# Kernel optimization log

Measured on AMD Instinct MI355X. Metric: run time of the kernel, lower is better.

Reference implementation:

```python
import jax, jax.numpy as jnp
import numpy as np

LATENT = 768
HEADS = 12
HEAD_DIM = LATENT // HEADS
FFN = 4 * LATENT


def setup_inputs() -> dict:
    key = jax.random.key(0)
    ks = jax.random.split(key, 16)
    s = 1.0 / np.sqrt(LATENT)
    inp = {
        "x": jax.random.normal(ks[0], (2, 2048, LATENT), dtype=jnp.float32),
        "Wq": jax.random.normal(ks[1], (LATENT, LATENT), dtype=jnp.float32) * s,
        "bq": jnp.zeros((LATENT,), jnp.float32),
        "Wk": jax.random.normal(ks[2], (LATENT, LATENT), dtype=jnp.float32) * s,
        "bk": jnp.zeros((LATENT,), jnp.float32),
        "Wv": jax.random.normal(ks[3], (LATENT, LATENT), dtype=jnp.float32) * s,
        "bv": jnp.zeros((LATENT,), jnp.float32),
        "Wo": jax.random.normal(ks[4], (LATENT, LATENT), dtype=jnp.float32) * s,
        "bo": jnp.zeros((LATENT,), jnp.float32),
        "ln1_g": jnp.ones((LATENT,), jnp.float32),
        "ln1_b": jnp.zeros((LATENT,), jnp.float32),
        "ln2_g": jnp.ones((LATENT,), jnp.float32),
        "ln2_b": jnp.zeros((LATENT,), jnp.float32),
        "W1": jax.random.normal(ks[5], (FFN, LATENT), dtype=jnp.float32) * s,
        "b1": jnp.zeros((FFN,), jnp.float32),
        "W2": jax.random.normal(ks[6], (LATENT, FFN), dtype=jnp.float32) * (1.0 / np.sqrt(FFN)),
        "b2": jnp.zeros((LATENT,), jnp.float32),
    }
    return inp


def _layernorm(x, g, b, eps=1e-5):
    mu = jnp.mean(x, axis=-1, keepdims=True)
    var = jnp.var(x, axis=-1, keepdims=True)
    return (x - mu) * jax.lax.rsqrt(var + eps) * g + b


def reference(x, Wq, bq, Wk, bk, Wv, bv, Wo, bo, ln1_g, ln1_b, ln2_g, ln2_b, W1, b1, W2, b2):
    b, n, d = x.shape
    # torch Linear: y = x @ W.T + bias
    Q = (x @ Wq.T + bq).reshape(b, n, HEADS, HEAD_DIM).transpose(0, 2, 1, 3)
    K = (x @ Wk.T + bk).reshape(b, n, HEADS, HEAD_DIM).transpose(0, 2, 1, 3)
    V = (x @ Wv.T + bv).reshape(b, n, HEADS, HEAD_DIM).transpose(0, 2, 1, 3)
    scores = jnp.einsum("bhqd,bhkd->bhqk", Q, K) / np.sqrt(HEAD_DIM)  # [b,h,n,n]
    weights = jax.nn.softmax(scores, axis=-1)
    attn = jnp.einsum("bhqk,bhkd->bhqd", weights, V)
    attn = attn.transpose(0, 2, 1, 3).reshape(b, n, d)
    attn = attn @ Wo.T + bo
    x = _layernorm(x + attn, ln1_g, ln1_b)
    h = jax.nn.gelu(x @ W1.T + b1, approximate=False)
    ffn = h @ W2.T + b2
    x = _layernorm(x + ffn, ln2_g, ln2_b)
    return x
```

## Files before the change

kernel.cpp:

```cpp
#include <hip/hip_runtime.h>
#include <hip/hip_bf16.h>
#include <cstddef>
#include <cstdint>

typedef __bf16 bf16_t;
typedef bf16_t bf16x8 __attribute__((ext_vector_type(8)));
typedef bf16_t bf16x4 __attribute__((ext_vector_type(4)));
typedef float f32x4 __attribute__((ext_vector_type(4)));

#define LATENT 768
#define FFN_DIM 3072
#define NTOK 4096
#define SEQ 2048
#define HEADS 12
#define HD 64

#define C2F 0.18033688011112042f

__device__ __forceinline__ void gload_lds16(const bf16_t* g, bf16_t* l) {
    __builtin_amdgcn_global_load_lds((const __attribute__((address_space(1))) void*)g,
                                     (__attribute__((address_space(3))) void*)l, 16, 0, 0);
}

struct CvtDesc {
    const float* src[7];
    bf16_t* dst[7];
    int n4[7];
    const float* bsrc[3];
    float* bdst;
};

__global__ __launch_bounds__(256) void cvt_f32_bf16(CvtDesc d) {
    int seg = blockIdx.y;
    if (seg == 7) {
        int which = blockIdx.x;
        if (which >= 3) return;
        int t = threadIdx.x;
#pragma unroll
        for (int i = 0; i < 3; ++i)
            d.bdst[which * LATENT + t + i * 256] = d.bsrc[which][t + i * 256];
        return;
    }
    int i = blockIdx.x * 256 + threadIdx.x;
    if (i >= d.n4[seg]) return;
    float4 v = ((const float4*)d.src[seg])[i];
    bf16x4 o;
    o[0] = (bf16_t)v.x; o[1] = (bf16_t)v.y; o[2] = (bf16_t)v.z; o[3] = (bf16_t)v.w;
    *(bf16x4*)&d.dst[seg][(size_t)i * 4] = o;
}

template<int EPI, int NT>
__global__ __launch_bounds__(256) void gemm128(const bf16_t* __restrict__ A,
                                               const bf16_t* __restrict__ B,
                                               const float* __restrict__ bias,
                                               void* __restrict__ Cv,
                                               int M, int N, int K) {
    __shared__ __align__(16) bf16_t As[2][128 * 32];
    __shared__ __align__(16) bf16_t Bs[2][NT * 32];
    int t = threadIdx.x;
    int w = t >> 6;
    int lane = t & 63, l16 = lane & 15, quad = lane >> 4;
    int xt = blockIdx.x + blockIdx.y;
    if (xt >= (int)gridDim.x) xt -= gridDim.x;
    int m0 = xt * 128, n0 = blockIdx.y * NT;
    int mrow0 = (w & 1) * 64, ncol0 = (w >> 1) * (NT / 2);
    const int NJ = NT / 32;

    f32x4 acc[4][NJ] = {};

    int srow = lane >> 2;
    int sseg = (lane & 3) * 8;

    auto stage = [&](int k0, int buf) {
        const bf16_t* Ag = A + (size_t)(m0 + w * 32 + srow) * K + k0 + sseg;
        gload_lds16(Ag,          &As[buf][(w * 32) * 32]);
        gload_lds16(Ag + 16 * K, &As[buf][(w * 32 + 16) * 32]);
        if (NT == 128) {
            const bf16_t* Bg = B + (size_t)(n0 + w * 32 + srow) * K + k0 + sseg;
            gload_lds16(Bg,          &Bs[buf][(w * 32) * 32]);
            gload_lds16(Bg + 16 * K, &Bs[buf][(w * 32 + 16) * 32]);
        } else {
            const bf16_t* Bg = B + (size_t)(n0 + w * 16 + srow) * K + k0 + sseg;
            gload_lds16(Bg, &Bs[buf][(w * 16) * 32]);
        }
    };

    int niter = K / 32;
    stage(0, 0);
    for (int kt = 0; kt < niter; ++kt) {
        __syncthreads();
        int cur = kt & 1;
        if (kt + 1 < niter) stage((kt + 1) * 32, cur ^ 1);

        bf16x8 a[4], b[NJ];
#pragma unroll
        for (int i = 0; i < 4; ++i)
            a[i] = *(const bf16x8*)&As[cur][(mrow0 + i * 16 + l16) * 32 + quad * 8];
#pragma unroll
        for (int j = 0; j < NJ; ++j)
            b[j] = *(const bf16x8*)&Bs[cur][(ncol0 + j * 16 + l16) * 32 + quad * 8];
#pragma unroll
        for (int i = 0; i < 4; ++i)
#pragma unroll
            for (int j = 0; j < NJ; ++j)
                acc[i][j] = __builtin_amdgcn_mfma_f32_16x16x32_bf16(a[i], b[j], acc[i][j], 0, 0, 0);
    }

    float* Cf = (float*)Cv;
    bf16_t* Cb = (bf16_t*)Cv;
#pragma unroll
    for (int j = 0; j < NJ; ++j) {
        int col = n0 + ncol0 + j * 16 + l16;
        float bvv = bias[col];
#pragma unroll
        for (int i = 0; i < 4; ++i) {
            int row0 = m0 + mrow0 + i * 16 + quad * 4;
#pragma unroll
            for (int r = 0; r < 4; ++r) {
                float v = acc[i][j][r] + bvv;
                if (EPI == 2) v = 0.5f * v * (1.0f + erff(v * 0.70710678118654752f));
                if (EPI == 3) { if (col < LATENT) v *= C2F; }
                if (EPI == 0) Cf[(size_t)(row0 + r) * N + col] = v;
                else          Cb[(size_t)(row0 + r) * N + col] = (bf16_t)v;
            }
        }
    }
}

template<int EPI>
__global__ __launch_bounds__(128) void gemm64(const bf16_t* __restrict__ A,
                                              const bf16_t* __restrict__ B,
                                              const float* __restrict__ bias,
                                              void* __restrict__ Cv,
                                              int M, int N, int K) {
    __shared__ __align__(16) bf16_t As[2][64 * 32];
    __shared__ __align__(16) bf16_t Bs[2][64 * 32];
    int t = threadIdx.x;
    int w = t >> 6;
    int lane = t & 63, l16 = lane & 15, quad = lane >> 4;
    int m0 = blockIdx.x * 64, n0 = blockIdx.y * 64;

    f32x4 acc[2][4] = {};

    int srow = lane >> 2;
    int sseg = (lane & 3) * 8;

    auto stage = [&](int k0, int buf) {
        const bf16_t* Ag = A + (size_t)(m0 + w * 32 + srow) * K + k0 + sseg;
        gload_lds16(Ag,          &As[buf][(w * 32) * 32]);
        gload_lds16(Ag + 16 * K, &As[buf][(w * 32 + 16) * 32]);
        const bf16_t* Bg = B + (size_t)(n0 + w * 32 + srow) * K + k0 + sseg;
        gload_lds16(Bg,          &Bs[buf][(w * 32) * 32]);
        gload_lds16(Bg + 16 * K, &Bs[buf][(w * 32 + 16) * 32]);
    };

    int niter = K / 32;
    stage(0, 0);
    for (int kt = 0; kt < niter; ++kt) {
        __syncthreads();
        int cur = kt & 1;
        if (kt + 1 < niter) stage((kt + 1) * 32, cur ^ 1);

        bf16x8 a[2], b[4];
#pragma unroll
        for (int i = 0; i < 2; ++i)
            a[i] = *(const bf16x8*)&As[cur][(w * 32 + i * 16 + l16) * 32 + quad * 8];
#pragma unroll
        for (int j = 0; j < 4; ++j)
            b[j] = *(const bf16x8*)&Bs[cur][(j * 16 + l16) * 32 + quad * 8];
#pragma unroll
        for (int i = 0; i < 2; ++i)
#pragma unroll
            for (int j = 0; j < 4; ++j)
                acc[i][j] = __builtin_amdgcn_mfma_f32_16x16x32_bf16(a[i], b[j], acc[i][j], 0, 0, 0);
    }

    float* Cf = (float*)Cv;
    bf16_t* Cb = (bf16_t*)Cv;
#pragma unroll
    for (int j = 0; j < 4; ++j) {
        int col = n0 + j * 16 + l16;
        float bvv = bias[col];
#pragma unroll
        for (int i = 0; i < 2; ++i) {
            int row0 = m0 + w * 32 + i * 16 + quad * 4;
#pragma unroll
            for (int r = 0; r < 4; ++r) {
                float v = acc[i][j][r] + bvv;
                if (EPI == 2) v = 0.5f * v * (1.0f + erff(v * 0.70710678118654752f));
                if (EPI == 0) Cf[(size_t)(row0 + r) * N + col] = v;
                else          Cb[(size_t)(row0 + r) * N + col] = (bf16_t)v;
            }
        }
    }
}

__global__ __launch_bounds__(256) void v_transpose(const bf16_t* __restrict__ QKV,
                                                   bf16_t* __restrict__ Vt) {
    __shared__ bf16_t Ts[64][68];
    int t = threadIdx.x;
    int bh = blockIdx.y;
    int b = bh / HEADS, h = bh % HEADS;
    int n0 = blockIdx.x * 64;
    size_t rowbase = (size_t)b * SEQ;
    int r = t >> 3, seg = (t & 7) * 8;
#pragma unroll
    for (int i = 0; i < 2; ++i) {
        int rr = r + i * 32;
        *(bf16x8*)&Ts[rr][seg] =
            *(const bf16x8*)&QKV[(rowbase + n0 + rr) * (3 * LATENT) + 2 * LATENT + h * HD + seg];
    }
    __syncthreads();
#pragma unroll
    for (int i = 0; i < 2; ++i) {
        int d = r + i * 32;
        bf16x8 o;
#pragma unroll
        for (int jj = 0; jj < 8; ++jj) o[jj] = Ts[seg + jj][d];
        *(bf16x8*)&Vt[((size_t)bh * HD + d) * SEQ + n0 + seg] = o;
    }
}

__global__ __launch_bounds__(256) void attn_flash(const bf16_t* __restrict__ QKV,
                                                  const bf16_t* __restrict__ Vt,
                                                  float* __restrict__ Op0,
                                                  float* __restrict__ Op1,
                                                  float* __restrict__ vs0,
                                                  float* __restrict__ vs1) {
    __shared__ __align__(16) bf16_t Ks[2][2][64][32];
    __shared__ __align__(16) bf16_t Vts[2][2][64][32];
    __shared__ __align__(16) bf16_t Ps[4][64][72];

    int t = threadIdx.x;
    int w = t >> 6;
    int lane = t & 63, l16 = lane & 15, quad = lane >> 4;
    int bh = blockIdx.x;
    int b = bh / HEADS, h = bh % HEADS;
    int qblk = blockIdx.y * 256;
    int z = blockIdx.z;
    float* Op = z ? Op1 : Op0;
    float* vs = z ? vs1 : vs0;
    size_t rowbase = (size_t)b * SEQ;
    int kbase = z * (SEQ / 2);
    const int LD = 3 * LATENT;
    int qw = qblk + w * 64;

    bf16x8 bq[4][2];
#pragma unroll
    for (int qt = 0; qt < 4; ++qt) {
        const bf16_t* qrow = QKV + (rowbase + qw + qt * 16 + l16) * LD + h * HD;
        bq[qt][0] = *(const bf16x8*)&qrow[quad * 8];
        bq[qt][1] = *(const bf16x8*)&qrow[32 + quad * 8];
    }

    f32x4 acc[4][4] = {};
    float vsum[4] = {};

    int srow = lane >> 2;
    int sseg = (lane & 3) * 8;

    {
        const bf16_t* kg = QKV + (rowbase + kbase + w * 16 + srow) * LD + LATENT + h * HD + sseg;
        gload_lds16(kg,      &Ks[0][0][w * 16][0]);
        gload_lds16(kg + 32, &Ks[0][1][w * 16][0]);
        const bf16_t* vg = Vt + ((size_t)bh * HD + w * 16 + srow) * SEQ + kbase + sseg;
        gload_lds16(vg,      &Vts[0][0][w * 16][0]);
        gload_lds16(vg + 32, &Vts[0][1][w * 16][0]);
    }

    for (int kt = 0; kt < SEQ / 128; ++kt) {
        __syncthreads();
        int cur = kt & 1;
        if (kt + 1 < SEQ / 128) {
            int nxt = cur ^ 1;
            int koff = kbase + (kt + 1) * 64;
            const bf16_t* kg = QKV + (rowbase + koff + w * 16 + srow) * LD + LATENT + h * HD + sseg;
            gload_lds16(kg,      &Ks[nxt][0][w * 16][0]);
            gload_lds16(kg + 32, &Ks[nxt][1][w * 16][0]);
            const bf16_t* vg = Vt + ((size_t)bh * HD + w * 16 + srow) * SEQ + koff + sseg;
            gload_lds16(vg,      &Vts[nxt][0][w * 16][0]);
            gload_lds16(vg + 32, &Vts[nxt][1][w * 16][0]);
        }

#pragma unroll
        for (int skt = 0; skt < 4; ++skt) {
            bf16x8 ak0 = *(const bf16x8*)&Ks[cur][0][skt * 16 + l16][quad * 8];
            bf16x8 ak1 = *(const bf16x8*)&Ks[cur][1][skt * 16 + l16][quad * 8];
#pragma unroll
            for (int qt = 0; qt < 4; ++qt) {
                f32x4 s = {};
                s = __builtin_amdgcn_mfma_f32_16x16x32_bf16(ak0, bq[qt][0], s, 0, 0, 0);
                s = __builtin_amdgcn_mfma_f32_16x16x32_bf16(ak1, bq[qt][1], s, 0, 0, 0);
                bf16x4 pk;
#pragma unroll
                for (int r = 0; r < 4; ++r) {
                    float p = __builtin_amdgcn_exp2f(s[r]);
                    vsum[qt] += p;
                    pk[r] = (bf16_t)p;
                }
                *(bf16x4*)&Ps[w][qt * 16 + l16][skt * 16 + quad * 4] = pk;
            }
        }
        __threadfence_block();

        bf16x8 bv[4][2];
#pragma unroll
        for (int dt = 0; dt < 4; ++dt) {
            bv[dt][0] = *(const bf16x8*)&Vts[cur][0][dt * 16 + l16][quad * 8];
            bv[dt][1] = *(const bf16x8*)&Vts[cur][1][dt * 16 + l16][quad * 8];
        }
#pragma unroll
        for (int qt = 0; qt < 4; ++qt) {
#pragma unroll
            for (int kc = 0; kc < 2; ++kc) {
                bf16x8 ap = *(const bf16x8*)&Ps[w][qt * 16 + l16][kc * 32 + quad * 8];
#pragma unroll
                for (int dt = 0; dt < 4; ++dt)
                    acc[qt][dt] = __builtin_amdgcn_mfma_f32_16x16x32_bf16(ap, bv[dt][kc], acc[qt][dt], 0, 0, 0);
            }
        }
    }

#pragma unroll
    for (int qt = 0; qt < 4; ++qt) {
        vsum[qt] += __shfl_xor(vsum[qt], 16, 64);
        vsum[qt] += __shfl_xor(vsum[qt], 32, 64);
        if (quad == 0)
            vs[(rowbase + qw + qt * 16 + l16) * HEADS + h] = vsum[qt];
    }

#pragma unroll
    for (int qt = 0; qt < 4; ++qt)
#pragma unroll
        for (int dt = 0; dt < 4; ++dt)
#pragma unroll
            for (int r = 0; r < 4; ++r) {
                size_t row = rowbase + qw + qt * 16 + quad * 4 + r;
                Op[row * LATENT + h * HD + dt * 16 + l16] = acc[qt][dt][r];
            }
}

__global__ __launch_bounds__(256) void attn_combine(const float* __restrict__ Op0,
                                                    const float* __restrict__ Op1,
                                                    const float* __restrict__ vs0,
                                                    const float* __restrict__ vs1,
                                                    bf16_t* __restrict__ O) {
    int row = blockIdx.x;
    int t = threadIdx.x;
    const float* a = Op0 + (size_t)row * LATENT;
    const float* bb = Op1 + (size_t)row * LATENT;
#pragma unroll
    for (int i = 0; i < 3; ++i) {
        int c = t + i * 256;
        int h = c >> 6;
        float denom = vs0[(size_t)row * HEADS + h] + vs1[(size_t)row * HEADS + h];
        O[(size_t)row * LATENT + c] = (bf16_t)((a[c] + bb[c]) / denom);
    }
}

__global__ __launch_bounds__(256) void ln_residual(const float* __restrict__ base,
                                                   const float* __restrict__ add,
                                                   const float* __restrict__ g,
                                                   const float* __restrict__ bta,
                                                   float* __restrict__ outf,
                                                   bf16_t* __restrict__ outb) {
    int row = blockIdx.x;
    const float* xr = base + (size_t)row * LATENT;
    const float* ar = add + (size_t)row * LATENT;
    int t = threadIdx.x;
    float v[3];
    float s = 0.f;
#pragma unroll
    for (int i = 0; i < 3; ++i) {
        v[i] = xr[t + i * 256] + ar[t + i * 256];
        s += v[i];
    }
    __shared__ float red[4];
#pragma unroll
    for (int off = 1; off < 64; off <<= 1) s += __shfl_xor(s, off, 64);
    if ((t & 63) == 0) red[t >> 6] = s;
    __syncthreads();
    float mu = (red[0] + red[1] + red[2] + red[3]) * (1.f / LATENT);
    float q = 0.f;
#pragma unroll
    for (int i = 0; i < 3; ++i) {
        float d = v[i] - mu;
        q += d * d;
    }
#pragma unroll
    for (int off = 1; off < 64; off <<= 1) q += __shfl_xor(q, off, 64);
    __syncthreads();
    if ((t & 63) == 0) red[t >> 6] = q;
    __syncthreads();
    float var = (red[0] + red[1] + red[2] + red[3]) * (1.f / LATENT);
    float rs = rsqrtf(var + 1e-5f);
#pragma unroll
    for (int i = 0; i < 3; ++i) {
        int cix = t + i * 256;
        float o = (v[i] - mu) * rs * g[cix] + bta[cix];
        outf[(size_t)row * LATENT + cix] = o;
        if (outb) outb[(size_t)row * LATENT + cix] = (bf16_t)o;
    }
}

extern "C" void kernel_launch(void* const* d_in, const int* in_sizes, int n_in,
                              void* d_out, int out_size, void* d_ws, size_t ws_size,
                              hipStream_t stream) {
    const float* x   = (const float*)d_in[0];
    const float* Wq  = (const float*)d_in[1];
    const float* bq  = (const float*)d_in[2];
    const float* Wk  = (const float*)d_in[3];
    const float* bk  = (const float*)d_in[4];
    const float* Wv  = (const float*)d_in[5];
    const float* bv  = (const float*)d_in[6];
    const float* Wo  = (const float*)d_in[7];
    const float* bo  = (const float*)d_in[8];
    const float* g1  = (const float*)d_in[9];
    const float* be1 = (const float*)d_in[10];
    const float* g2  = (const float*)d_in[11];
    const float* be2 = (const float*)d_in[12];
    const float* W1  = (const float*)d_in[13];
    const float* b1  = (const float*)d_in[14];
    const float* W2  = (const float*)d_in[15];
    const float* b2  = (const float*)d_in[16];
    float* out = (float*)d_out;

    char* ws = (char*)d_ws;
    size_t off = 0;
    auto alloc = [&](size_t bytes) {
        char* p = ws + off;
        off = (off + bytes + 255) & ~(size_t)255;
        return p;
    };
    bf16_t* xbf   = (bf16_t*)alloc((size_t)NTOK * LATENT * 2);
    bf16_t* Wcat  = (bf16_t*)alloc((size_t)3 * LATENT * LATENT * 2);
    bf16_t* Wobf  = (bf16_t*)alloc((size_t)LATENT * LATENT * 2);
    bf16_t* W1bf  = (bf16_t*)alloc((size_t)FFN_DIM * LATENT * 2);
    bf16_t* W2bf  = (bf16_t*)alloc((size_t)LATENT * FFN_DIM * 2);
    float*  bcat  = (float*)alloc((size_t)3 * LATENT * 4);
    bf16_t* QKV   = (bf16_t*)alloc((size_t)NTOK * 3 * LATENT * 2);
    bf16_t* attnO = (bf16_t*)alloc((size_t)NTOK * LATENT * 2);
    float*  tmpf  = (float*)alloc((size_t)NTOK * LATENT * 4);
    float*  y1f   = (float*)alloc((size_t)NTOK * LATENT * 4);
    bf16_t* y1bf  = (bf16_t*)alloc((size_t)NTOK * LATENT * 2);
    bf16_t* hbf   = (bf16_t*)alloc((size_t)NTOK * FFN_DIM * 2);
    float*  vsa   = (float*)alloc((size_t)NTOK * HEADS * 4);
    float*  vsb   = (float*)alloc((size_t)NTOK * HEADS * 4);
    bf16_t* Vtg   = (bf16_t*)hbf;
    float*  Oa    = tmpf;
    float*  Ob    = y1f;

    CvtDesc cd;
    cd.src[0] = x;   cd.dst[0] = xbf;                        cd.n4[0] = NTOK * LATENT / 4;
    cd.src[1] = Wq;  cd.dst[1] = Wcat;                       cd.n4[1] = LATENT * LATENT / 4;
    cd.src[2] = Wk;  cd.dst[2] = Wcat + LATENT * LATENT;     cd.n4[2] = LATENT * LATENT / 4;
    cd.src[3] = Wv;  cd.dst[3] = Wcat + 2 * LATENT * LATENT; cd.n4[3] = LATENT * LATENT / 4;
    cd.src[4] = Wo;  cd.dst[4] = Wobf;                       cd.n4[4] = LATENT * LATENT / 4;
    cd.src[5] = W1;  cd.dst[5] = W1bf;                       cd.n4[5] = FFN_DIM * LATENT / 4;
    cd.src[6] = W2;  cd.dst[6] = W2bf;                       cd.n4[6] = FFN_DIM * LATENT / 4;
    cd.bsrc[0] = bq; cd.bsrc[1] = bk; cd.bsrc[2] = bv;
    cd.bdst = bcat;
    {
        int maxn4 = NTOK * LATENT / 4;
        dim3 grid((maxn4 + 255) / 256, 8);
        cvt_f32_bf16<<<grid, 256, 0, stream>>>(cd);
    }

    gemm128<3, 128><<<dim3(NTOK / 128, 3 * LATENT / 128), 256, 0, stream>>>(
        xbf, Wcat, bcat, QKV, NTOK, 3 * LATENT, LATENT);

    v_transpose<<<dim3(SEQ / 64, 2 * HEADS), 256, 0, stream>>>(QKV, Vtg);

    attn_flash<<<dim3(2 * HEADS, SEQ / 256, 2), 256, 0, stream>>>(QKV, Vtg, Oa, Ob, vsa, vsb);

    attn_combine<<<NTOK, 256, 0, stream>>>(Oa, Ob, vsa, vsb, attnO);

    gemm64<0><<<dim3(NTOK / 64, LATENT / 64), 128, 0, stream>>>(
        attnO, Wobf, bo, tmpf, NTOK, LATENT, LATENT);

    ln_residual<<<NTOK, 256, 0, stream>>>(x, tmpf, g1, be1, y1f, y1bf);

    gemm128<2, 128><<<dim3(NTOK / 128, FFN_DIM / 128), 256, 0, stream>>>(
        y1bf, W1bf, b1, hbf, NTOK, FFN_DIM, LATENT);

    gemm64<0><<<dim3(NTOK / 64, LATENT / 64), 128, 0, stream>>>(
        hbf, W2bf, b2, tmpf, NTOK, LATENT, FFN_DIM);

    ln_residual<<<NTOK, 256, 0, stream>>>(y1f, tmpf, g2, be2, out, nullptr);
}
```

Before: 311.0 us.

## Double wavefronts per block in GEMMs and halve attention query tile

The 128x128 GEMM now runs 8 waves per block (512 threads), each owning a 64x32 sub-tile, and the 64x64 GEMM runs 4 waves, each owning 32x32. Staging is spread over more waves, so each wave issues one load per operand. The flash-attention kernel drops from 256 to 128 query rows per block, with 32 rows per wave, which doubles the grid. The aim is more waves in flight and fewer accumulator registers per wave to hide latency, at the cost of less register-level reuse per wave and more LDS reads per MFMA.

```diff
diff --git a/kernel.cpp b/kernel.cpp
--- a/kernel.cpp
+++ b/kernel.cpp
@@ -49,40 +49,33 @@
     *(bf16x4*)&d.dst[seg][(size_t)i * 4] = o;
 }
 
-template<int EPI, int NT>
-__global__ __launch_bounds__(256) void gemm128(const bf16_t* __restrict__ A,
+template<int EPI>
+__global__ __launch_bounds__(512) void gemm128(const bf16_t* __restrict__ A,
                                                const bf16_t* __restrict__ B,
                                                const float* __restrict__ bias,
                                                void* __restrict__ Cv,
                                                int M, int N, int K) {
     __shared__ __align__(16) bf16_t As[2][128 * 32];
-    __shared__ __align__(16) bf16_t Bs[2][NT * 32];
+    __shared__ __align__(16) bf16_t Bs[2][128 * 32];
     int t = threadIdx.x;
     int w = t >> 6;
     int lane = t & 63, l16 = lane & 15, quad = lane >> 4;
     int xt = blockIdx.x + blockIdx.y;
     if (xt >= (int)gridDim.x) xt -= gridDim.x;
-    int m0 = xt * 128, n0 = blockIdx.y * NT;
-    int mrow0 = (w & 1) * 64, ncol0 = (w >> 1) * (NT / 2);
-    const int NJ = NT / 32;
-
-    f32x4 acc[4][NJ] = {};
+    int m0 = xt * 128, n0 = blockIdx.y * 128;
+    int wm = w & 1, wn = w >> 1;
+    int mrow0 = wm * 64, ncol0 = wn * 32;
+
+    f32x4 acc[4][2] = {};
 
     int srow = lane >> 2;
     int sseg = (lane & 3) * 8;
 
     auto stage = [&](int k0, int buf) {
-        const bf16_t* Ag = A + (size_t)(m0 + w * 32 + srow) * K + k0 + sseg;
-        gload_lds16(Ag,          &As[buf][(w * 32) * 32]);
-        gload_lds16(Ag + 16 * K, &As[buf][(w * 32 + 16) * 32]);
-        if (NT == 128) {
-            const bf16_t* Bg = B + (size_t)(n0 + w * 32 + srow) * K + k0 + sseg;
-            gload_lds16(Bg,          &Bs[buf][(w * 32) * 32]);
-            gload_lds16(Bg + 16 * K, &Bs[buf][(w * 32 + 16) * 32]);
-        } else {
-            const bf16_t* Bg = B + (size_t)(n0 + w * 16 + srow) * K + k0 + sseg;
-            gload_lds16(Bg, &Bs[buf][(w * 16) * 32]);
-        }
+        const bf16_t* Ag = A + (size_t)(m0 + w * 16 + srow) * K + k0 + sseg;
+        gload_lds16(Ag, &As[buf][(w * 16) * 32]);
+        const bf16_t* Bg = B + (size_t)(n0 + w * 16 + srow) * K + k0 + sseg;
+        gload_lds16(Bg, &Bs[buf][(w * 16) * 32]);
     };
 
     int niter = K / 32;
@@ -92,24 +85,24 @@
         int cur = kt & 1;
         if (kt + 1 < niter) stage((kt + 1) * 32, cur ^ 1);
 
-        bf16x8 a[4], b[NJ];
+        bf16x8 a[4], b[2];
 #pragma unroll
         for (int i = 0; i < 4; ++i)
             a[i] = *(const bf16x8*)&As[cur][(mrow0 + i * 16 + l16) * 32 + quad * 8];
 #pragma unroll
-        for (int j = 0; j < NJ; ++j)
+        for (int j = 0; j < 2; ++j)
             b[j] = *(const bf16x8*)&Bs[cur][(ncol0 + j * 16 + l16) * 32 + quad * 8];
 #pragma unroll
         for (int i = 0; i < 4; ++i)
 #pragma unroll
-            for (int j = 0; j < NJ; ++j)
+            for (int j = 0; j < 2; ++j)
                 acc[i][j] = __builtin_amdgcn_mfma_f32_16x16x32_bf16(a[i], b[j], acc[i][j], 0, 0, 0);
     }
 
     float* Cf = (float*)Cv;
     bf16_t* Cb = (bf16_t*)Cv;
 #pragma unroll
-    for (int j = 0; j < NJ; ++j) {
+    for (int j = 0; j < 2; ++j) {
         int col = n0 + ncol0 + j * 16 + l16;
         float bvv = bias[col];
 #pragma unroll
@@ -128,7 +121,7 @@
 }
 
 template<int EPI>
-__global__ __launch_bounds__(128) void gemm64(const bf16_t* __restrict__ A,
+__global__ __launch_bounds__(256) void gemm64(const bf16_t* __restrict__ A,
                                               const bf16_t* __restrict__ B,
                                               const float* __restrict__ bias,
                                               void* __restrict__ Cv,
@@ -139,19 +132,18 @@
     int w = t >> 6;
     int lane = t & 63, l16 = lane & 15, quad = lane >> 4;
     int m0 = blockIdx.x * 64, n0 = blockIdx.y * 64;
-
-    f32x4 acc[2][4] = {};
+    int wm = w & 1, wn = w >> 1;
+
+    f32x4 acc[2][2] = {};
 
     int srow = lane >> 2;
     int sseg = (lane & 3) * 8;
 
     auto stage = [&](int k0, int buf) {
-        const bf16_t* Ag = A + (size_t)(m0 + w * 32 + srow) * K + k0 + sseg;
-        gload_lds16(Ag,          &As[buf][(w * 32) * 32]);
-        gload_lds16(Ag + 16 * K, &As[buf][(w * 32 + 16) * 32]);
-        const bf16_t* Bg = B + (size_t)(n0 + w * 32 + srow) * K + k0 + sseg;
-        gload_lds16(Bg,          &Bs[buf][(w * 32) * 32]);
-        gload_lds16(Bg + 16 * K, &Bs[buf][(w * 32 + 16) * 32]);
+        const bf16_t* Ag = A + (size_t)(m0 + w * 16 + srow) * K + k0 + sseg;
+        gload_lds16(Ag, &As[buf][(w * 16) * 32]);
+        const bf16_t* Bg = B + (size_t)(n0 + w * 16 + srow) * K + k0 + sseg;
+        gload_lds16(Bg, &Bs[buf][(w * 16) * 32]);
     };
 
     int niter = K / 32;
@@ -161,29 +153,29 @@
         int cur = kt & 1;
         if (kt + 1 < niter) stage((kt + 1) * 32, cur ^ 1);
 
-        bf16x8 a[2], b[4];
+        bf16x8 a[2], b[2];
 #pragma unroll
         for (int i = 0; i < 2; ++i)
-            a[i] = *(const bf16x8*)&As[cur][(w * 32 + i * 16 + l16) * 32 + quad * 8];
-#pragma unroll
-        for (int j = 0; j < 4; ++j)
-            b[j] = *(const bf16x8*)&Bs[cur][(j * 16 + l16) * 32 + quad * 8];
+            a[i] = *(const bf16x8*)&As[cur][(wm * 32 + i * 16 + l16) * 32 + quad * 8];
+#pragma unroll
+        for (int j = 0; j < 2; ++j)
+            b[j] = *(const bf16x8*)&Bs[cur][(wn * 32 + j * 16 + l16) * 32 + quad * 8];
 #pragma unroll
         for (int i = 0; i < 2; ++i)
 #pragma unroll
-            for (int j = 0; j < 4; ++j)
+            for (int j = 0; j < 2; ++j)
                 acc[i][j] = __builtin_amdgcn_mfma_f32_16x16x32_bf16(a[i], b[j], acc[i][j], 0, 0, 0);
     }
 
     float* Cf = (float*)Cv;
     bf16_t* Cb = (bf16_t*)Cv;
 #pragma unroll
-    for (int j = 0; j < 4; ++j) {
-        int col = n0 + j * 16 + l16;
+    for (int j = 0; j < 2; ++j) {
+        int col = n0 + wn * 32 + j * 16 + l16;
         float bvv = bias[col];
 #pragma unroll
         for (int i = 0; i < 2; ++i) {
-            int row0 = m0 + w * 32 + i * 16 + quad * 4;
+            int row0 = m0 + wm * 32 + i * 16 + quad * 4;
 #pragma unroll
             for (int r = 0; r < 4; ++r) {
                 float v = acc[i][j][r] + bvv;
@@ -229,32 +221,32 @@
                                                   float* __restrict__ vs1) {
     __shared__ __align__(16) bf16_t Ks[2][2][64][32];
     __shared__ __align__(16) bf16_t Vts[2][2][64][32];
-    __shared__ __align__(16) bf16_t Ps[4][64][72];
+    __shared__ __align__(16) bf16_t Ps[4][32][72];
 
     int t = threadIdx.x;
     int w = t >> 6;
     int lane = t & 63, l16 = lane & 15, quad = lane >> 4;
     int bh = blockIdx.x;
     int b = bh / HEADS, h = bh % HEADS;
-    int qblk = blockIdx.y * 256;
+    int qblk = blockIdx.y * 128;
     int z = blockIdx.z;
     float* Op = z ? Op1 : Op0;
     float* vs = z ? vs1 : vs0;
     size_t rowbase = (size_t)b * SEQ;
     int kbase = z * (SEQ / 2);
     const int LD = 3 * LATENT;
-    int qw = qblk + w * 64;
-
-    bf16x8 bq[4][2];
-#pragma unroll
-    for (int qt = 0; qt < 4; ++qt) {
+    int qw = qblk + w * 32;
+
+    bf16x8 bq[2][2];
+#pragma unroll
+    for (int qt = 0; qt < 2; ++qt) {
         const bf16_t* qrow = QKV + (rowbase + qw + qt * 16 + l16) * LD + h * HD;
         bq[qt][0] = *(const bf16x8*)&qrow[quad * 8];
         bq[qt][1] = *(const bf16x8*)&qrow[32 + quad * 8];
     }
 
-    f32x4 acc[4][4] = {};
-    float vsum[4] = {};
+    f32x4 acc[2][4] = {};
+    float vsum[2] = {};
 
     int srow = lane >> 2;
     int sseg = (lane & 3) * 8;
@@ -287,7 +279,7 @@
             bf16x8 ak0 = *(const bf16x8*)&Ks[cur][0][skt * 16 + l16][quad * 8];
             bf16x8 ak1 = *(const bf16x8*)&Ks[cur][1][skt * 16 + l16][quad * 8];
 #pragma unroll
-            for (int qt = 0; qt < 4; ++qt) {
+            for (int qt = 0; qt < 2; ++qt) {
                 f32x4 s = {};
                 s = __builtin_amdgcn_mfma_f32_16x16x32_bf16(ak0, bq[qt][0], s, 0, 0, 0);
                 s = __builtin_amdgcn_mfma_f32_16x16x32_bf16(ak1, bq[qt][1], s, 0, 0, 0);
@@ -310,7 +302,7 @@
             bv[dt][1] = *(const bf16x8*)&Vts[cur][1][dt * 16 + l16][quad * 8];
         }
 #pragma unroll
-        for (int qt = 0; qt < 4; ++qt) {
+        for (int qt = 0; qt < 2; ++qt) {
 #pragma unroll
             for (int kc = 0; kc < 2; ++kc) {
                 bf16x8 ap = *(const bf16x8*)&Ps[w][qt * 16 + l16][kc * 32 + quad * 8];
@@ -322,7 +314,7 @@
     }
 
 #pragma unroll
-    for (int qt = 0; qt < 4; ++qt) {
+    for (int qt = 0; qt < 2; ++qt) {
         vsum[qt] += __shfl_xor(vsum[qt], 16, 64);
         vsum[qt] += __shfl_xor(vsum[qt], 32, 64);
         if (quad == 0)
@@ -330,7 +322,7 @@
     }
 
 #pragma unroll
-    for (int qt = 0; qt < 4; ++qt)
+    for (int qt = 0; qt < 2; ++qt)
 #pragma unroll
         for (int dt = 0; dt < 4; ++dt)
 #pragma unroll
@@ -466,24 +458,24 @@
         cvt_f32_bf16<<<grid, 256, 0, stream>>>(cd);
     }
 
-    gemm128<3, 128><<<dim3(NTOK / 128, 3 * LATENT / 128), 256, 0, stream>>>(
+    gemm128<3><<<dim3(NTOK / 128, 3 * LATENT / 128), 512, 0, stream>>>(
         xbf, Wcat, bcat, QKV, NTOK, 3 * LATENT, LATENT);
 
     v_transpose<<<dim3(SEQ / 64, 2 * HEADS), 256, 0, stream>>>(QKV, Vtg);
 
-    attn_flash<<<dim3(2 * HEADS, SEQ / 256, 2), 256, 0, stream>>>(QKV, Vtg, Oa, Ob, vsa, vsb);
+    attn_flash<<<dim3(2 * HEADS, SEQ / 128, 2), 256, 0, stream>>>(QKV, Vtg, Oa, Ob, vsa, vsb);
 
     attn_combine<<<NTOK, 256, 0, stream>>>(Oa, Ob, vsa, vsb, attnO);
 
-    gemm64<0><<<dim3(NTOK / 64, LATENT / 64), 128, 0, stream>>>(
+    gemm64<0><<<dim3(NTOK / 64, LATENT / 64), 256, 0, stream>>>(
         attnO, Wobf, bo, tmpf, NTOK, LATENT, LATENT);
 
     ln_residual<<<NTOK, 256, 0, stream>>>(x, tmpf, g1, be1, y1f, y1bf);
 
-    gemm128<2, 128><<<dim3(NTOK / 128, FFN_DIM / 128), 256, 0, stream>>>(
+    gemm128<2><<<dim3(NTOK / 128, FFN_DIM / 128), 512, 0, stream>>>(
         y1bf, W1bf, b1, hbf, NTOK, FFN_DIM, LATENT);
 
-    gemm64<0><<<dim3(NTOK / 64, LATENT / 64), 128, 0, stream>>>(
+    gemm64<0><<<dim3(NTOK / 64, LATENT / 64), 256, 0, stream>>>(
         hbf, W2bf, b2, tmpf, NTOK, LATENT, FFN_DIM);
 
     ln_residual<<<NTOK, 256, 0, stream>>>(y1f, tmpf, g2, be2, out, nullptr);
```

New measurement: 302.1 us. 1.03x faster.
